# Kernel optimization log

Measured on AMD Instinct MI355X. Metric: run time of the kernel, lower is better.

## Reference

```python
import jax, jax.numpy as jnp
import numpy as np

B, S, D, H, DFF = 8, 1024, 1024, 16, 4096
DK = D // H
EPS = 1e-6
NEG = -1e9


def _layer_norm(x, gamma, beta):
    # Faithful to hand-rolled LN: torch std is unbiased (ddof=1), eps added to sigma.
    mu = jnp.mean(x, axis=-1, keepdims=True)
    sigma = jnp.std(x, axis=-1, keepdims=True, ddof=1)
    return gamma * (x - mu) / (EPS + sigma) + beta


def setup_inputs() -> dict:
    key = jax.random.key(0)
    ks = jax.random.split(key, 12)
    s = 0.02
    inp = {
        "x": jax.random.normal(ks[0], (B, S, D), dtype=jnp.float32),
        "src_mask": jnp.ones((B, 1, 1, S), dtype=jnp.int32),
        "Wq": jax.random.normal(ks[1], (D, D), dtype=jnp.float32) * s,
        "bq": jnp.zeros((D,), dtype=jnp.float32),
        "Wk": jax.random.normal(ks[2], (D, D), dtype=jnp.float32) * s,
        "bk": jnp.zeros((D,), dtype=jnp.float32),
        "Wv": jax.random.normal(ks[3], (D, D), dtype=jnp.float32) * s,
        "bv": jnp.zeros((D,), dtype=jnp.float32),
        "Wo": jax.random.normal(ks[4], (D, D), dtype=jnp.float32) * s,
        "bo": jnp.zeros((D,), dtype=jnp.float32),
        "W1": jax.random.normal(ks[5], (DFF, D), dtype=jnp.float32) * s,
        "b1": jnp.zeros((DFF,), dtype=jnp.float32),
        "W2": jax.random.normal(ks[6], (D, DFF), dtype=jnp.float32) * s,
        "b2": jnp.zeros((D,), dtype=jnp.float32),
        "g1": jnp.ones((1,), dtype=jnp.float32),
        "be1": jnp.zeros((1,), dtype=jnp.float32),
        "g2": jnp.ones((1,), dtype=jnp.float32),
        "be2": jnp.zeros((1,), dtype=jnp.float32),
    }
    return inp


def _encoder_block(x, src_mask, Wq, bq, Wk, bk, Wv, bv, Wo, bo,
                   W1, b1, W2, b2, g1, be1, g2, be2):
    # Multi-head self-attention (dropout = identity in eval)
    def split(h):  # [B,S,D] -> [B,H,S,DK]
        return h.reshape(B, S, H, DK).transpose(0, 2, 1, 3)

    q = split(x @ Wq.T + bq)
    k = split(x @ Wk.T + bk)
    v = split(x @ Wv.T + bv)

    scores = jnp.einsum("bhqd,bhkd->bhqk", q, k) / jnp.sqrt(jnp.float32(DK))
    scores = jnp.where(src_mask == 0, NEG, scores)
    probs = jax.nn.softmax(scores, axis=-1)
    attn = jnp.einsum("bhqk,bhkd->bhqd", probs, v)
    attn = attn.transpose(0, 2, 1, 3).reshape(B, S, D)
    attn = attn @ Wo.T + bo

    x1 = _layer_norm(x + attn, g1, be1)

    ff = jax.nn.relu(x1 @ W1.T + b1) @ W2.T + b2
    x2 = _layer_norm(x1 + ff, g2, be2)
    return x2


def reference(x, src_mask, Wq, bq, Wk, bk, Wv, bv, Wo, bo,
              W1, b1, W2, b2, g1, be1, g2, be2):
    return _encoder_block(x, src_mask, Wq, bq, Wk, bk, Wv, bv, Wo, bo,
                          W1, b1, W2, b2, g1, be1, g2, be2)
```

## Files before the change

kernel.cpp:

```cpp
#include <hip/hip_runtime.h>
#include <stdint.h>

#define BB 8
#define SS 1024
#define DD 1024
#define HH 16
#define DFF 4096
#define MT (BB*SS)

typedef __attribute__((ext_vector_type(8))) short bf16x8;
typedef __attribute__((ext_vector_type(4))) short s16x4;
typedef __attribute__((ext_vector_type(4))) float f32x4;
typedef __attribute__((ext_vector_type(16))) float f32x16;
typedef unsigned int u32x2 __attribute__((ext_vector_type(2)));

#define LOG2E 1.44269504088896340736f

__device__ __forceinline__ short f2bf(float f) {
  union { float f; uint32_t u; } v; v.f = f;
  uint32_t r = v.u + 0x7FFFu + ((v.u >> 16) & 1u);
  return (short)(r >> 16);
}

__device__ __forceinline__ void gload_lds16(const void* g, void* l) {
  __builtin_amdgcn_global_load_lds(
      (__attribute__((address_space(1))) uint32_t*)(uintptr_t)g,
      (__attribute__((address_space(3))) uint32_t*)(uint32_t)(uintptr_t)l,
      16, 0, 0);
}

__device__ __forceinline__ uint32_t cvtpk(float lo, float hi) {
  uint32_t r;
  asm("v_cvt_pk_bf16_f32 %0, %1, %2" : "=v"(r) : "v"(lo), "v"(hi));
  return r;
}

__device__ __forceinline__ void swap2(uint32_t a, uint32_t b, uint32_t& x, uint32_t& y) {
#if __has_builtin(__builtin_amdgcn_permlane32_swap)
  u32x2 r = __builtin_amdgcn_permlane32_swap(a, b, false, false);
  x = r.x; y = r.y;
#else
  uint32_t asw = (uint32_t)__shfl_xor((int)a, 32, 64);
  uint32_t bsw = (uint32_t)__shfl_xor((int)b, 32, 64);
  bool h = (threadIdx.x & 32) != 0;
  x = h ? bsw : a;
  y = h ? b : asw;
#endif
}

__global__ __launch_bounds__(256) void cvt_bf16(const float* __restrict__ in,
                                                short* __restrict__ out, int n8) {
  int i = blockIdx.x * 256 + threadIdx.x;
  if (i >= n8) return;
  f32x4 a = *(const f32x4*)(in + (size_t)i * 8);
  f32x4 b = *(const f32x4*)(in + (size_t)i * 8 + 4);
  bf16x8 o;
  o[0]=f2bf(a[0]); o[1]=f2bf(a[1]); o[2]=f2bf(a[2]); o[3]=f2bf(a[3]);
  o[4]=f2bf(b[0]); o[5]=f2bf(b[1]); o[6]=f2bf(b[2]); o[7]=f2bf(b[3]);
  *(bf16x8*)(out + (size_t)i * 8) = o;
}

template<int BM, int RELU, int RES, int OUTF, int OUTB, int QKV, int SPLITK>
__global__ __launch_bounds__(512, 2) void gemm_ring(
    const short* __restrict__ A, const short* __restrict__ W,
    const float* __restrict__ bq, const float* __restrict__ bk,
    const float* __restrict__ bv, const float* __restrict__ res,
    float* __restrict__ outF, short* __restrict__ outB,
    int M, int N, int K, int Kc, float qscale)
{
  constexpr int AISS   = BM / 128;
  constexpr int SLOT_A = BM * 32 * 2;
  constexpr int SLOT   = SLOT_A + 256 * 32 * 2;
  constexpr int MI     = BM / 32;
  __shared__ __align__(16) char lds[3 * SLOT];

  const int tid = threadIdx.x, lane = tid & 63, wid = tid >> 6;
  const int wm = wid >> 2, wn = wid & 3;
  const int lrow = lane & 15, lk = lane >> 4;

  const int nwg = gridDim.x;
  const int cpx = nwg >> 3;
  const int id  = blockIdx.x;
  const int wg  = (id & 7) * cpx + (id >> 3);
  const int gx  = N >> 8;
  const int bx  = wg % gx, by = wg / gx;
  const int row0 = by * BM, col0 = bx * 256;
  const int koff = SPLITK ? blockIdx.z * Kc : 0;

  const int lineo = lane >> 3;
  const int rin   = lineo * 2 + ((lane >> 2) & 1);
  const int ksrc  = (lane & 3) ^ (lineo & 3);

  const short* Asrc[AISS];
#pragma unroll
  for (int j = 0; j < AISS; ++j)
    Asrc[j] = A + (size_t)(row0 + (wid * AISS + j) * 16 + rin) * K + koff + ksrc * 8;
  const short* Bsrc[2];
#pragma unroll
  for (int j = 0; j < 2; ++j)
    Bsrc[j] = W + (size_t)(col0 + (wid * 2 + j) * 16 + rin) * K + koff + ksrc * 8;

  const f32x4 z4 = {0.f, 0.f, 0.f, 0.f};
  f32x4 acc[MI][4];
#pragma unroll
  for (int i = 0; i < MI; ++i)
#pragma unroll
    for (int j = 0; j < 4; ++j) acc[i][j] = z4;

  const int NT = Kc >> 5;

  auto stage = [&](int ts, int s) {
    char* base = lds + s * SLOT;
    int ko = ts * 32;
#pragma unroll
    for (int j = 0; j < AISS; ++j)
      gload_lds16(Asrc[j] + ko, base + (wid * AISS + j) * 1024);
#pragma unroll
    for (int j = 0; j < 2; ++j)
      gload_lds16(Bsrc[j] + ko, base + SLOT_A + (wid * 2 + j) * 1024);
  };

  stage(0, 0);
  stage(1, 1);

  const int laneterm = (lrow >> 1) * 128 + (lrow & 1) * 64 + ((lk ^ ((lrow >> 1) & 3)) * 16);

  int sr = 0;
  for (int t = 0; t < NT; ++t) {
    const int sw = (sr == 0) ? 2 : sr - 1;
    const int ts = (t + 2 < NT) ? t + 2 : NT - 1;
    stage(ts, sw);
    if (AISS == 2) asm volatile("s_waitcnt vmcnt(8)" ::: "memory");
    else           asm volatile("s_waitcnt vmcnt(6)" ::: "memory");
    __builtin_amdgcn_s_barrier();
    __builtin_amdgcn_sched_barrier(0);

    const char* As = lds + sr * SLOT;
    const char* Bs = As + SLOT_A;
    bf16x8 af[MI], bfr[4];
#pragma unroll
    for (int mi = 0; mi < MI; ++mi)
      af[mi] = *(const bf16x8*)(As + wm * (BM * 32) + mi * 1024 + laneterm);
#pragma unroll
    for (int ni = 0; ni < 4; ++ni)
      bfr[ni] = *(const bf16x8*)(Bs + wn * 4096 + ni * 1024 + laneterm);

    __builtin_amdgcn_s_setprio(1);
#pragma unroll
    for (int mi = 0; mi < MI; ++mi)
#pragma unroll
      for (int ni = 0; ni < 4; ++ni)
        acc[mi][ni] = __builtin_amdgcn_mfma_f32_16x16x32_bf16(af[mi], bfr[ni], acc[mi][ni], 0, 0, 0);
    __builtin_amdgcn_s_setprio(0);

    __builtin_amdgcn_s_barrier();
    sr = (sr == 2) ? 0 : sr + 1;
  }

  const int sel    = QKV ? (col0 >> 10) : 0;
  const float* bias = QKV ? (sel == 0 ? bq : (sel == 1 ? bk : bv)) : bq;
  const int strideN = QKV ? 1024 : N;
  short* outBp = OUTB ? (outB + (QKV ? (size_t)sel * MT * DD : 0)) : outB;
  const float scl = (QKV && sel == 0) ? qscale : 1.f;

#pragma unroll
  for (int mi = 0; mi < MI; ++mi) {
#pragma unroll
    for (int ni = 0; ni < 4; ++ni) {
      int col  = col0 + wn * 64 + ni * 16 + lrow;
      int coll = QKV ? (col & 1023) : col;
      float bvv = SPLITK ? 0.f : bias[coll];
#pragma unroll
      for (int r = 0; r < 4; ++r) {
        int row = row0 + wm * (BM / 2) + mi * 16 + lk * 4 + r;
        float v = acc[mi][ni][r] + bvv;
        if (QKV) v *= scl;
        if (RELU) v = fmaxf(v, 0.f);
        size_t idx = (size_t)row * strideN + coll;
        if (SPLITK) {
          atomicAdd(&outF[idx], v);
        } else {
          if (RES)  v += res[idx];
          if (OUTF) outF[idx] = v;
          if (OUTB) outBp[idx] = f2bf(v);
        }
      }
    }
  }
}

__global__ __launch_bounds__(256) void transpose_v(const short* __restrict__ Vb,
                                                   short* __restrict__ Vt) {
  const int s = blockIdx.x * 256 + threadIdx.x;
  const int u = blockIdx.y;
  const int bh = blockIdx.z, b = bh >> 4, h = bh & 15;
  bf16x8 v = *(const bf16x8*)(Vb + ((size_t)(b * SS + s)) * DD + h * 64 + u * 8);
  size_t ob = ((size_t)bh * 64 + u * 8) * SS + s;
#pragma unroll
  for (int j = 0; j < 8; ++j) Vt[ob + (size_t)j * SS] = v[j];
}

__global__ __launch_bounds__(256) void attn_flash3(
    const short* __restrict__ Qm, const short* __restrict__ Km,
    const short* __restrict__ Vtg, const int* __restrict__ mask,
    short* __restrict__ Om)
{
  __shared__ short KsB[2 * 64 * 64];
  __shared__ short VsB[2 * 64 * 64];
  __shared__ float ma_all[SS];
  __shared__ float fb[4 * 32];

  const int tid = threadIdx.x, lane = tid & 63, wid = tid >> 6;
  const int l31 = lane & 31, hi = lane >> 5;
  const int bh = blockIdx.y, b = bh >> 4, h = bh & 15;
  const int q0 = blockIdx.x * 128 + wid * 32;

  {
    const int* mrow = mask + b * SS;
#pragma unroll
    for (int i = 0; i < 4; ++i) {
      int idx = i * 256 + tid;
      ma_all[idx] = (mrow[idx] == 0) ? -1.442695e9f : 0.f;
    }
  }

  bf16x8 qf[4];
  {
    const short* qrow = Qm + ((size_t)(b * SS + q0 + l31)) * DD + h * 64;
#pragma unroll
    for (int t = 0; t < 4; ++t) qf[t] = *(const bf16x8*)(qrow + t * 16 + hi * 8);
  }

  f32x16 acc0, acc1;
#pragma unroll
  for (int i = 0; i < 16; ++i) { acc0[i] = 0.f; acc1[i] = 0.f; }
  float m_r = -3e38f, l_r = 0.f;

  const int srow = tid >> 3;
  const int su = tid & 7;

  auto stageKV = [&](int kt2, int bi) {
#pragma unroll
    for (int i = 0; i < 2; ++i) {
      int r = i * 32 + srow;
      int uu = su ^ (r & 7);
      gload_lds16(Km + ((size_t)(b * SS + kt2 + r)) * DD + h * 64 + uu * 8,
                  KsB + bi * 4096 + (i * 256 + wid * 64) * 8);
      gload_lds16(Vtg + ((size_t)(bh * 64 + r)) * SS + kt2 + uu * 8,
                  VsB + bi * 4096 + (i * 256 + wid * 64) * 8);
    }
  };

  __syncthreads();
  stageKV(0, 0);

  for (int t = 0; t < 16; ++t) {
    if (t < 15) {
      stageKV((t + 1) << 6, (t + 1) & 1);
      asm volatile("s_waitcnt vmcnt(4)" ::: "memory");
    } else {
      asm volatile("s_waitcnt vmcnt(0)" ::: "memory");
    }
    __builtin_amdgcn_s_barrier();
    __builtin_amdgcn_sched_barrier(0);

    const short* Ks = KsB + (t & 1) * 4096;
    const short* Vs = VsB + (t & 1) * 4096;

    f32x16 s0, s1;
#pragma unroll
    for (int i = 0; i < 16; ++i) { s0[i] = 0.f; s1[i] = 0.f; }
#pragma unroll
    for (int t4 = 0; t4 < 4; ++t4) {
      int u = (t4 * 2 + hi) ^ (l31 & 7);
      bf16x8 k0 = *(const bf16x8*)(Ks + l31 * 64 + u * 8);
      bf16x8 k1 = *(const bf16x8*)(Ks + (32 + l31) * 64 + u * 8);
      s0 = __builtin_amdgcn_mfma_f32_32x32x16_bf16(k0, qf[t4], s0, 0, 0, 0);
      s1 = __builtin_amdgcn_mfma_f32_32x32x16_bf16(k1, qf[t4], s1, 0, 0, 0);
    }

    const float* map = ma_all + (t << 6);
    float p0[16], p1[16];
    float mx = -3e38f;
#pragma unroll
    for (int g = 0; g < 4; ++g) {
      f32x4 a0 = *(const f32x4*)(map + g * 8 + hi * 4);
      f32x4 a1 = *(const f32x4*)(map + 32 + g * 8 + hi * 4);
#pragma unroll
      for (int j = 0; j < 4; ++j) {
        float v0 = s0[g * 4 + j] + a0[j];
        float v1 = s1[g * 4 + j] + a1[j];
        p0[g * 4 + j] = v0; p1[g * 4 + j] = v1;
        mx = fmaxf(mx, fmaxf(v0, v1));
      }
    }
    mx = fmaxf(mx, __shfl_xor(mx, 32, 64));

    if (!__all(mx <= m_r + 8.f)) {
      float mn  = fmaxf(m_r, mx);
      float fac = exp2f(m_r - mn);
      m_r = mn;
      l_r *= fac;
      fb[wid * 32 + l31] = fac;
#pragma unroll
      for (int g = 0; g < 4; ++g) {
        f32x4 fv = *(const f32x4*)(fb + wid * 32 + g * 8 + hi * 4);
#pragma unroll
        for (int j = 0; j < 4; ++j) { acc0[g * 4 + j] *= fv[j]; acc1[g * 4 + j] *= fv[j]; }
      }
    }

    float rs = 0.f;
#pragma unroll
    for (int r = 0; r < 16; ++r) {
      p0[r] = exp2f(p0[r] - m_r);
      p1[r] = exp2f(p1[r] - m_r);
      rs += p0[r] + p1[r];
    }
    rs += __shfl_xor(rs, 32, 64);
    l_r += rs;

    uint32_t w0[8], w1[8];
#pragma unroll
    for (int m = 0; m < 8; ++m) {
      w0[m] = cvtpk(p0[2 * m], p0[2 * m + 1]);
      w1[m] = cvtpk(p1[2 * m], p1[2 * m + 1]);
    }
    uint32_t pa[4][4];
    swap2(w0[0], w0[2], pa[0][0], pa[0][2]);
    swap2(w0[1], w0[3], pa[0][1], pa[0][3]);
    swap2(w0[4], w0[6], pa[1][0], pa[1][2]);
    swap2(w0[5], w0[7], pa[1][1], pa[1][3]);
    swap2(w1[0], w1[2], pa[2][0], pa[2][2]);
    swap2(w1[1], w1[3], pa[2][1], pa[2][3]);
    swap2(w1[4], w1[6], pa[3][0], pa[3][2]);
    swap2(w1[5], w1[7], pa[3][1], pa[3][3]);

#pragma unroll
    for (int kc = 0; kc < 4; ++kc) {
      union { uint32_t w[4]; bf16x8 v; } pu;
      pu.w[0] = pa[kc][0]; pu.w[1] = pa[kc][1]; pu.w[2] = pa[kc][2]; pu.w[3] = pa[kc][3];
      int u = (kc * 2 + hi) ^ (l31 & 7);
      bf16x8 v0 = *(const bf16x8*)(Vs + l31 * 64 + u * 8);
      bf16x8 v1 = *(const bf16x8*)(Vs + (32 + l31) * 64 + u * 8);
      acc0 = __builtin_amdgcn_mfma_f32_32x32x16_bf16(pu.v, v0, acc0, 0, 0, 0);
      acc1 = __builtin_amdgcn_mfma_f32_32x32x16_bf16(pu.v, v1, acc1, 0, 0, 0);
    }

    __builtin_amdgcn_s_barrier();
  }

  fb[wid * 32 + l31] = 1.f / l_r;
#pragma unroll
  for (int g = 0; g < 4; ++g) {
    f32x4 rv = *(const f32x4*)(fb + wid * 32 + g * 8 + hi * 4);
#pragma unroll
    for (int j = 0; j < 4; ++j) {
      int q = q0 + g * 8 + hi * 4 + j;
      size_t base = ((size_t)(b * SS + q)) * DD + h * 64 + l31;
      Om[base]      = f2bf(acc0[g * 4 + j] * rv[j]);
      Om[base + 32] = f2bf(acc1[g * 4 + j] * rv[j]);
    }
  }
}

template<int WRITE_BF16>
__global__ __launch_bounds__(256) void layernorm_k(
    float* __restrict__ x, short* __restrict__ xb,
    const float* __restrict__ g, const float* __restrict__ be)
{
  const int row = blockIdx.x, tid = threadIdx.x;
  float* xr = x + (size_t)row * DD;
  f32x4 a = *(const f32x4*)(xr + tid * 4);
  float s  = a[0] + a[1] + a[2] + a[3];
  float ss = a[0]*a[0] + a[1]*a[1] + a[2]*a[2] + a[3]*a[3];
#pragma unroll
  for (int o = 1; o < 64; o <<= 1) { s += __shfl_xor(s, o, 64); ss += __shfl_xor(ss, o, 64); }
  __shared__ float red[8];
  const int wid = tid >> 6, lane = tid & 63;
  if (lane == 0) { red[wid] = s; red[4 + wid] = ss; }
  __syncthreads();
  s  = red[0] + red[1] + red[2] + red[3];
  ss = red[4] + red[5] + red[6] + red[7];
  float mu  = s * (1.f / DD);
  float var = fmaxf((ss - (float)DD * mu * mu) * (1.f / (DD - 1)), 0.f);
  float inv = g[0] / (1e-6f + sqrtf(var));
  float bb  = be[0];
#pragma unroll
  for (int j = 0; j < 4; ++j) a[j] = (a[j] - mu) * inv + bb;
  *(f32x4*)(xr + tid * 4) = a;
  if (WRITE_BF16) {
    s16x4 o;
#pragma unroll
    for (int j = 0; j < 4; ++j) o[j] = f2bf(a[j]);
    *(s16x4*)(xb + (size_t)row * DD + tid * 4) = o;
  }
}

__global__ __launch_bounds__(256) void ln2_combine(
    const float* __restrict__ P, const float* __restrict__ x1,
    const float* __restrict__ b2, const float* __restrict__ g,
    const float* __restrict__ be, float* __restrict__ out)
{
  const int row = blockIdx.x, tid = threadIdx.x;
  f32x4 a  = *(const f32x4*)(P  + (size_t)row * DD + tid * 4);
  f32x4 xr = *(const f32x4*)(x1 + (size_t)row * DD + tid * 4);
  f32x4 bb4 = *(const f32x4*)(b2 + tid * 4);
#pragma unroll
  for (int j = 0; j < 4; ++j) a[j] = a[j] + bb4[j] + xr[j];
  float s  = a[0] + a[1] + a[2] + a[3];
  float ss = a[0]*a[0] + a[1]*a[1] + a[2]*a[2] + a[3]*a[3];
#pragma unroll
  for (int o = 1; o < 64; o <<= 1) { s += __shfl_xor(s, o, 64); ss += __shfl_xor(ss, o, 64); }
  __shared__ float red[8];
  const int wid = tid >> 6, lane = tid & 63;
  if (lane == 0) { red[wid] = s; red[4 + wid] = ss; }
  __syncthreads();
  s  = red[0] + red[1] + red[2] + red[3];
  ss = red[4] + red[5] + red[6] + red[7];
  float mu  = s * (1.f / DD);
  float var = fmaxf((ss - (float)DD * mu * mu) * (1.f / (DD - 1)), 0.f);
  float inv = g[0] / (1e-6f + sqrtf(var));
  float bb  = be[0];
#pragma unroll
  for (int j = 0; j < 4; ++j) a[j] = (a[j] - mu) * inv + bb;
  *(f32x4*)(out + (size_t)row * DD + tid * 4) = a;
}

extern "C" void kernel_launch(void* const* d_in, const int* in_sizes, int n_in,
                              void* d_out, int out_size, void* d_ws, size_t ws_size,
                              hipStream_t stream) {
  const float* x    = (const float*)d_in[0];
  const int*   mask = (const int*)d_in[1];
  const float* Wq = (const float*)d_in[2];  const float* bq = (const float*)d_in[3];
  const float* Wk = (const float*)d_in[4];  const float* bk = (const float*)d_in[5];
  const float* Wv = (const float*)d_in[6];  const float* bv = (const float*)d_in[7];
  const float* Wo = (const float*)d_in[8];  const float* bo = (const float*)d_in[9];
  const float* W1 = (const float*)d_in[10]; const float* b1 = (const float*)d_in[11];
  const float* W2 = (const float*)d_in[12]; const float* b2 = (const float*)d_in[13];
  const float* g1 = (const float*)d_in[14]; const float* be1 = (const float*)d_in[15];
  const float* g2 = (const float*)d_in[16]; const float* be2 = (const float*)d_in[17];
  float* out = (float*)d_out;

  char* ws = (char*)d_ws;
  size_t off = 0;
  auto alloc = [&](size_t bytes) -> char* {
    char* p = ws + off; off += (bytes + 255) & ~(size_t)255; return p;
  };
  short* xb  = (short*)alloc((size_t)MT * DD * 2);
  short* wqb = (short*)alloc((size_t)DD * DD * 2);
  short* wkb = (short*)alloc((size_t)DD * DD * 2);
  short* wvb = (short*)alloc((size_t)DD * DD * 2);
  short* wob = (short*)alloc((size_t)DD * DD * 2);
  short* w1b = (short*)alloc((size_t)DFF * DD * 2);
  short* w2b = (short*)alloc((size_t)DD * DFF * 2);
  short* Qb  = (short*)alloc((size_t)MT * DD * 2);
  short* Kb  = (short*)alloc((size_t)MT * DD * 2);
  short* Vb  = (short*)alloc((size_t)MT * DD * 2);
  short* Ab  = (short*)alloc((size_t)MT * DD * 2);
  float* x1  = (float*)alloc((size_t)MT * DD * 4);
  short* F1  = Qb;
  short* x1b = xb;
  short* Vt  = (short*)x1;
  float* P0  = (float*)ws;
  (void)wkb; (void)wvb; (void)Kb; (void)Vb;

  const float qscale = 0.125f * LOG2E;

  cvt_bf16<<<(MT * DD / 8 + 255) / 256, 256, 0, stream>>>(x, xb, MT * DD / 8);
  cvt_bf16<<<(DD * DD / 8 + 255) / 256, 256, 0, stream>>>(Wq, wqb, DD * DD / 8);
  cvt_bf16<<<(DD * DD / 8 + 255) / 256, 256, 0, stream>>>(Wk, wkb, DD * DD / 8);
  cvt_bf16<<<(DD * DD / 8 + 255) / 256, 256, 0, stream>>>(Wv, wvb, DD * DD / 8);
  cvt_bf16<<<(DD * DD / 8 + 255) / 256, 256, 0, stream>>>(Wo, wob, DD * DD / 8);
  cvt_bf16<<<(DFF * DD / 8 + 255) / 256, 256, 0, stream>>>(W1, w1b, DFF * DD / 8);
  cvt_bf16<<<(DD * DFF / 8 + 255) / 256, 256, 0, stream>>>(W2, w2b, DD * DFF / 8);

  gemm_ring<128,0,0,0,1,1,0><<<dim3((3072/256)*(MT/128)), 512, 0, stream>>>(
      xb, wqb, bq, bk, bv, nullptr, nullptr, Qb, MT, 3072, DD, DD, qscale);

  transpose_v<<<dim3(SS/256, 8, BB*HH), 256, 0, stream>>>(Vb, Vt);
  attn_flash3<<<dim3(SS/128, BB*HH), 256, 0, stream>>>(Qb, Kb, Vt, mask, Ab);

  gemm_ring<128,0,1,1,0,0,0><<<dim3((DD/256)*(MT/128)), 512, 0, stream>>>(
      Ab, wob, bo, bo, bo, x, x1, nullptr, MT, DD, DD, DD, 1.f);
  layernorm_k<1><<<MT, 256, 0, stream>>>(x1, x1b, g1, be1);

  gemm_ring<128,1,0,0,1,0,0><<<dim3((DFF/256)*(MT/128)), 512, 0, stream>>>(
      x1b, w1b, b1, b1, b1, nullptr, nullptr, F1, MT, DFF, DD, DD, 1.f);

  hipMemsetAsync(P0, 0, (size_t)MT * DD * 4, stream);
  gemm_ring<128,0,0,1,0,0,1><<<dim3((DD/256)*(MT/128), 1, 2), 512, 0, stream>>>(
      F1, w2b, b2, b2, b2, nullptr, P0, nullptr, MT, DD, DFF, DFF/2, 1.f);
  ln2_combine<<<MT, 256, 0, stream>>>(P0, x1, b2, g2, be2, out);
}
```

Measured before the change: 425.6 us.

## Merge weight conversions, enlarge GEMM tiles, replace split-K atomics with bf16 partials

```diff
diff --git a/kernel.cpp b/kernel.cpp
--- a/kernel.cpp
+++ b/kernel.cpp
@@ -20,6 +20,9 @@
   union { float f; uint32_t u; } v; v.f = f;
   uint32_t r = v.u + 0x7FFFu + ((v.u >> 16) & 1u);
   return (short)(r >> 16);
+}
+__device__ __forceinline__ float bf2f(short s) {
+  union { uint32_t u; float f; } v; v.u = ((uint32_t)(uint16_t)s) << 16; return v.f;
 }
 
 __device__ __forceinline__ void gload_lds16(const void* g, void* l) {
@@ -58,6 +61,24 @@
   o[0]=f2bf(a[0]); o[1]=f2bf(a[1]); o[2]=f2bf(a[2]); o[3]=f2bf(a[3]);
   o[4]=f2bf(b[0]); o[5]=f2bf(b[1]); o[6]=f2bf(b[2]); o[7]=f2bf(b[3]);
   *(bf16x8*)(out + (size_t)i * 8) = o;
+}
+
+struct WCvt { const float* s[6]; short* d[6]; };
+__global__ __launch_bounds__(256) void cvt_weights(WCvt w) {
+  int u = blockIdx.x * 256 + threadIdx.x;
+  if (u >= 1572864) return;
+  int sel; int base;
+  if      (u <  524288) { sel = u >> 17;            base = (u & 131071); }
+  else if (u < 1048576) { sel = 4;                  base = u - 524288; }
+  else                  { sel = 5;                  base = u - 1048576; }
+  const float* in = w.s[sel] + (size_t)base * 8;
+  short* out = w.d[sel] + (size_t)base * 8;
+  f32x4 a = *(const f32x4*)(in);
+  f32x4 b = *(const f32x4*)(in + 4);
+  bf16x8 o;
+  o[0]=f2bf(a[0]); o[1]=f2bf(a[1]); o[2]=f2bf(a[2]); o[3]=f2bf(a[3]);
+  o[4]=f2bf(b[0]); o[5]=f2bf(b[1]); o[6]=f2bf(b[2]); o[7]=f2bf(b[3]);
+  *(bf16x8*)(out) = o;
 }
 
 template<int BM, int RELU, int RES, int OUTF, int OUTB, int QKV, int SPLITK>
@@ -160,7 +181,8 @@
   const int sel    = QKV ? (col0 >> 10) : 0;
   const float* bias = QKV ? (sel == 0 ? bq : (sel == 1 ? bk : bv)) : bq;
   const int strideN = QKV ? 1024 : N;
-  short* outBp = OUTB ? (outB + (QKV ? (size_t)sel * MT * DD : 0)) : outB;
+  short* outBp = OUTB ? (outB + (QKV ? (size_t)sel * MT * DD : 0)
+                              + (SPLITK ? (size_t)blockIdx.z * M * strideN : 0)) : outB;
   const float scl = (QKV && sel == 0) ? qscale : 1.f;
 
 #pragma unroll
@@ -177,13 +199,9 @@
         if (QKV) v *= scl;
         if (RELU) v = fmaxf(v, 0.f);
         size_t idx = (size_t)row * strideN + coll;
-        if (SPLITK) {
-          atomicAdd(&outF[idx], v);
-        } else {
-          if (RES)  v += res[idx];
-          if (OUTF) outF[idx] = v;
-          if (OUTB) outBp[idx] = f2bf(v);
-        }
+        if (RES)  v += res[idx];
+        if (OUTF) outF[idx] = v;
+        if (OUTB) outBp[idx] = f2bf(v);
       }
     }
   }
@@ -398,16 +416,19 @@
 }
 
 __global__ __launch_bounds__(256) void ln2_combine(
-    const float* __restrict__ P, const float* __restrict__ x1,
-    const float* __restrict__ b2, const float* __restrict__ g,
-    const float* __restrict__ be, float* __restrict__ out)
+    const short* __restrict__ P0, const short* __restrict__ P1,
+    const float* __restrict__ x1, const float* __restrict__ b2,
+    const float* __restrict__ g, const float* __restrict__ be,
+    float* __restrict__ out)
 {
   const int row = blockIdx.x, tid = threadIdx.x;
-  f32x4 a  = *(const f32x4*)(P  + (size_t)row * DD + tid * 4);
+  s16x4 pa = *(const s16x4*)(P0 + (size_t)row * DD + tid * 4);
+  s16x4 pb = *(const s16x4*)(P1 + (size_t)row * DD + tid * 4);
   f32x4 xr = *(const f32x4*)(x1 + (size_t)row * DD + tid * 4);
   f32x4 bb4 = *(const f32x4*)(b2 + tid * 4);
-#pragma unroll
-  for (int j = 0; j < 4; ++j) a[j] = a[j] + bb4[j] + xr[j];
+  f32x4 a;
+#pragma unroll
+  for (int j = 0; j < 4; ++j) a[j] = bf2f(pa[j]) + bf2f(pb[j]) + bb4[j] + xr[j];
   float s  = a[0] + a[1] + a[2] + a[3];
   float ss = a[0]*a[0] + a[1]*a[1] + a[2]*a[2] + a[3]*a[3];
 #pragma unroll
@@ -462,20 +483,18 @@
   short* F1  = Qb;
   short* x1b = xb;
   short* Vt  = (short*)x1;
-  float* P0  = (float*)ws;
+  short* P01 = (short*)ws;
   (void)wkb; (void)wvb; (void)Kb; (void)Vb;
 
   const float qscale = 0.125f * LOG2E;
 
   cvt_bf16<<<(MT * DD / 8 + 255) / 256, 256, 0, stream>>>(x, xb, MT * DD / 8);
-  cvt_bf16<<<(DD * DD / 8 + 255) / 256, 256, 0, stream>>>(Wq, wqb, DD * DD / 8);
-  cvt_bf16<<<(DD * DD / 8 + 255) / 256, 256, 0, stream>>>(Wk, wkb, DD * DD / 8);
-  cvt_bf16<<<(DD * DD / 8 + 255) / 256, 256, 0, stream>>>(Wv, wvb, DD * DD / 8);
-  cvt_bf16<<<(DD * DD / 8 + 255) / 256, 256, 0, stream>>>(Wo, wob, DD * DD / 8);
-  cvt_bf16<<<(DFF * DD / 8 + 255) / 256, 256, 0, stream>>>(W1, w1b, DFF * DD / 8);
-  cvt_bf16<<<(DD * DFF / 8 + 255) / 256, 256, 0, stream>>>(W2, w2b, DD * DFF / 8);
-
-  gemm_ring<128,0,0,0,1,1,0><<<dim3((3072/256)*(MT/128)), 512, 0, stream>>>(
+  WCvt wc;
+  wc.s[0] = Wq; wc.s[1] = Wk; wc.s[2] = Wv; wc.s[3] = Wo; wc.s[4] = W1; wc.s[5] = W2;
+  wc.d[0] = wqb; wc.d[1] = wkb; wc.d[2] = wvb; wc.d[3] = wob; wc.d[4] = w1b; wc.d[5] = w2b;
+  cvt_weights<<<(1572864 + 255) / 256, 256, 0, stream>>>(wc);
+
+  gemm_ring<256,0,0,0,1,1,0><<<dim3((3072/256)*(MT/256)), 512, 0, stream>>>(
       xb, wqb, bq, bk, bv, nullptr, nullptr, Qb, MT, 3072, DD, DD, qscale);
 
   transpose_v<<<dim3(SS/256, 8, BB*HH), 256, 0, stream>>>(Vb, Vt);
@@ -485,11 +504,10 @@
       Ab, wob, bo, bo, bo, x, x1, nullptr, MT, DD, DD, DD, 1.f);
   layernorm_k<1><<<MT, 256, 0, stream>>>(x1, x1b, g1, be1);
 
-  gemm_ring<128,1,0,0,1,0,0><<<dim3((DFF/256)*(MT/128)), 512, 0, stream>>>(
+  gemm_ring<256,1,0,0,1,0,0><<<dim3((DFF/256)*(MT/256)), 512, 0, stream>>>(
       x1b, w1b, b1, b1, b1, nullptr, nullptr, F1, MT, DFF, DD, DD, 1.f);
 
-  hipMemsetAsync(P0, 0, (size_t)MT * DD * 4, stream);
-  gemm_ring<128,0,0,1,0,0,1><<<dim3((DD/256)*(MT/128), 1, 2), 512, 0, stream>>>(
-      F1, w2b, b2, b2, b2, nullptr, P0, nullptr, MT, DD, DFF, DFF/2, 1.f);
-  ln2_combine<<<MT, 256, 0, stream>>>(P0, x1, b2, g2, be2, out);
-}
+  gemm_ring<256,0,0,0,1,0,1><<<dim3((DD/256)*(MT/256), 1, 2), 512, 0, stream>>>(
+      F1, w2b, b2, b2, b2, nullptr, nullptr, P01, MT, DD, DFF, DFF/2, 1.f);
+  ln2_combine<<<MT, 256, 0, stream>>>(P01, P01 + (size_t)MT * DD, x1, b2, g2, be2, out);
+}
```

After: 375.0 us. 11.9% less time.
